# Kernel tuning notes

Measured on AMD Instinct MI355X. Metric: run time of the kernel, lower is better.

The kernel has to match this reference:

```python
import jax, jax.numpy as jnp
import numpy as np
import math

NUM_HEADS = 16
HEAD_SIZE = 64
BLOCK = 64          # SLA block size for pooled block scores / sparse selection
TOPK_RATIO = 0.1    # fraction of KV blocks attended per query block


def setup_inputs() -> dict:
    key = jax.random.key(0)
    kq, kk, kv = jax.random.split(key, 3)
    B, S, HD = 2, 4096, NUM_HEADS * HEAD_SIZE
    return {
        "query": jax.random.normal(kq, (B, S, HD), dtype=jnp.float32),
        "key": jax.random.normal(kk, (B, S, HD), dtype=jnp.float32),
        "value": jax.random.normal(kv, (B, S, HD), dtype=jnp.float32),
    }


def _sla_attention(q, k, v):
    # q, k, v: (B, H, S, D). Block-topk sparse attention (SLA-style):
    # mean-pool q/k per block, score blocks, keep top-k key blocks per
    # query block, gather only those K/V blocks, softmax over them.
    B, H, S, D = q.shape
    Nb = S // BLOCK
    scale = 1.0 / math.sqrt(D)

    qb = q.reshape(B, H, Nb, BLOCK, D)
    kb = k.reshape(B, H, Nb, BLOCK, D)
    vb = v.reshape(B, H, Nb, BLOCK, D)

    q_pool = qb.mean(axis=3)  # (B,H,Nb,D)
    k_pool = kb.mean(axis=3)  # (B,H,Nb,D)
    block_scores = jnp.einsum("bhid,bhjd->bhij", q_pool, k_pool) * scale

    K = max(1, int(math.ceil(TOPK_RATIO * Nb)))
    _, idx = jax.lax.top_k(block_scores, K)  # (B,H,Nb,K) selected key blocks

    # Gather selected key/value blocks: (B,H,Nb,K,BLOCK,D)
    gather_idx = idx[..., None, None]
    k_sel = jnp.take_along_axis(kb[:, :, None], gather_idx, axis=3)
    v_sel = jnp.take_along_axis(vb[:, :, None], gather_idx, axis=3)

    # Per-query-block scores over the K*BLOCK selected keys
    scores = jnp.einsum("bhnqd,bhnkjd->bhnqkj", qb, k_sel) * scale
    scores = scores.reshape(B, H, Nb, BLOCK, K * BLOCK)
    probs = jax.nn.softmax(scores, axis=-1)

    v_flat = v_sel.reshape(B, H, Nb, K * BLOCK, D)
    out = jnp.einsum("bhnqk,bhnkd->bhnqd", probs, v_flat)
    return out.reshape(B, H, S, D)


def reference(query, key, value):
    B, S, HD = query.shape
    H, D = NUM_HEADS, HEAD_SIZE
    # b s (h d) -> b h s d
    q = query.reshape(B, S, H, D).transpose(0, 2, 1, 3)
    k = key.reshape(B, S, H, D).transpose(0, 2, 1, 3)
    v = value.reshape(B, S, H, D).transpose(0, 2, 1, 3)
    out = _sla_attention(q, k, v)  # (B,H,S,D)
    # b h s d -> b s (h d)
    return out.transpose(0, 2, 1, 3).reshape(B, S, HD)
```

## Files before the change

### kernel.cpp

```cpp
#include <hip/hip_runtime.h>

constexpr int Bn = 2;
constexpr int Sn = 4096;
constexpr int Hh = 16;
constexpr int Dn = 64;
constexpr int HD = 1024;
constexpr int NB = 64;
constexpr int KS = 7;

typedef _Float16 f16x8 __attribute__((ext_vector_type(8)));
typedef _Float16 f16x4 __attribute__((ext_vector_type(4)));
typedef float    f32x4 __attribute__((ext_vector_type(4)));

static __device__ __forceinline__ f16x4 cvt4(float4 v) {
    f16x4 r;
    r[0] = (_Float16)v.x; r[1] = (_Float16)v.y;
    r[2] = (_Float16)v.z; r[3] = (_Float16)v.w;
    return r;
}
static __device__ __forceinline__ f16x8 cvt8(float4 a, float4 b) {
    f16x8 r;
    r[0] = (_Float16)a.x; r[1] = (_Float16)a.y;
    r[2] = (_Float16)a.z; r[3] = (_Float16)a.w;
    r[4] = (_Float16)b.x; r[5] = (_Float16)b.y;
    r[6] = (_Float16)b.z; r[7] = (_Float16)b.w;
    return r;
}

__global__ __launch_bounds__(64) void sla_pool(const float* __restrict__ Q,
                                               const float* __restrict__ K,
                                               float* __restrict__ qpool,
                                               float* __restrict__ kpool) {
    int bid = blockIdx.x;
    int b   = bid / (Hh * NB);
    int rem = bid % (Hh * NB);
    int h   = rem / NB;
    int nb  = rem % NB;
    int d   = threadIdx.x;

    const float* qp = Q + ((size_t)b * Sn + (size_t)nb * 64) * HD + h * Dn + d;
    const float* kp = K + ((size_t)b * Sn + (size_t)nb * 64) * HD + h * Dn + d;
    double sq = 0.0, sk = 0.0;
    #pragma unroll 16
    for (int r = 0; r < 64; ++r) {
        sq += (double)qp[(size_t)r * HD];
        sk += (double)kp[(size_t)r * HD];
    }
    qpool[(size_t)bid * 64 + d] = (float)(sq * (1.0 / 64.0));
    kpool[(size_t)bid * 64 + d] = (float)(sk * (1.0 / 64.0));
}

__global__ __launch_bounds__(64) void sla_topk(const float* __restrict__ qpool,
                                               const float* __restrict__ kpool,
                                               int* __restrict__ topk) {
    int bid = blockIdx.x;
    int bh  = bid / NB;
    int j   = threadIdx.x;

    const float* qp = qpool + (size_t)bid * 64;
    const float* kp = kpool + ((size_t)bh * NB + j) * 64;
    double s = 0.0;
    #pragma unroll 8
    for (int d = 0; d < 64; ++d) s += (double)qp[d] * (double)kp[d];

    double v  = s;
    int   idx = j;
    #pragma unroll
    for (int it = 0; it < KS; ++it) {
        double bv = v; int bi = idx;
        #pragma unroll
        for (int off = 1; off < 64; off <<= 1) {
            double ov = __shfl_xor(bv, off);
            int    oi = __shfl_xor(bi, off);
            if (ov > bv || (ov == bv && oi < bi)) { bv = ov; bi = oi; }
        }
        if (j == 0) topk[(size_t)bid * KS + it] = bi;
        if (idx == bi) v = -1e300;
    }
}

__global__ __launch_bounds__(256) void sla_attn(const float* __restrict__ Q,
                                                const float* __restrict__ K,
                                                const float* __restrict__ V,
                                                const int* __restrict__ topk,
                                                float* __restrict__ O) {
    __shared__ _Float16 Ks[64][64];
    __shared__ _Float16 Vt[64][72];
    __shared__ _Float16 Pq[4][16][68];

    int raw = blockIdx.x;
    int bid = (raw & 7) * 256 + (raw >> 3);

    int b   = bid / (Hh * NB);
    int rem = bid % (Hh * NB);
    int h   = rem / NB;
    int nb  = rem % NB;

    int tid  = threadIdx.x;
    int w    = tid >> 6;
    int lane = tid & 63;
    int c    = lane & 15;
    int g    = lane >> 4;

    int skey = tid >> 2;
    int sd3  = tid & 3;
    int sdg  = sd3 << 4;
    int vcol = skey ^ (sd3 << 4);
    int kch0 = ((sd3 << 1) + 0) ^ (skey & 7);
    int kch1 = ((sd3 << 1) + 1) ^ (skey & 7);
    int rch0 = (g + 0) ^ (c & 7);
    int rch1 = (g + 4) ^ (c & 7);

    int jidx[KS];
    {
        const int* tkp = topk + (size_t)bid * KS;
        #pragma unroll
        for (int i = 0; i < KS; ++i) jidx[i] = tkp[i];
    }

    f16x8 qf[2];
    {
        const float* qrow = Q + ((size_t)b * Sn + (size_t)nb * 64 + w * 16 + c) * HD + h * Dn;
        #pragma unroll
        for (int s2 = 0; s2 < 2; ++s2) {
            float4 a0 = *(const float4*)(qrow + s2 * 32 + g * 8);
            float4 a1 = *(const float4*)(qrow + s2 * 32 + g * 8 + 4);
            f16x8 q;
            q[0] = (_Float16)(a0.x * 0.125f); q[1] = (_Float16)(a0.y * 0.125f);
            q[2] = (_Float16)(a0.z * 0.125f); q[3] = (_Float16)(a0.w * 0.125f);
            q[4] = (_Float16)(a1.x * 0.125f); q[5] = (_Float16)(a1.y * 0.125f);
            q[6] = (_Float16)(a1.z * 0.125f); q[7] = (_Float16)(a1.w * 0.125f);
            qf[s2] = q;
        }
    }

    float m = -1e30f, l = 0.f;
    f32x4 oacc[4];
    #pragma unroll
    for (int t = 0; t < 4; ++t) oacc[t] = f32x4{0.f, 0.f, 0.f, 0.f};

    const float* kbase = K + (size_t)b * Sn * HD + h * Dn;
    const float* vbase = V + (size_t)b * Sn * HD + h * Dn;

    float4 kx[4], vx[4];
    {
        const float* kp = kbase + ((size_t)jidx[0] * 64 + skey) * HD + sdg;
        const float* vp = vbase + ((size_t)jidx[0] * 64 + skey) * HD + sdg;
        #pragma unroll
        for (int i = 0; i < 4; ++i) kx[i] = *(const float4*)(kp + i * 4);
        #pragma unroll
        for (int i = 0; i < 4; ++i) vx[i] = *(const float4*)(vp + i * 4);
    }

    for (int kb = 0; kb < KS; ++kb) {
        __syncthreads();
        *(f16x8*)&Ks[skey][kch0 * 8] = cvt8(kx[0], kx[1]);
        *(f16x8*)&Ks[skey][kch1 * 8] = cvt8(kx[2], kx[3]);
        #pragma unroll
        for (int i = 0; i < 4; ++i) {
            float4 v = vx[i];
            int db = sdg + i * 4;
            Vt[db + 0][vcol] = (_Float16)v.x;
            Vt[db + 1][vcol] = (_Float16)v.y;
            Vt[db + 2][vcol] = (_Float16)v.z;
            Vt[db + 3][vcol] = (_Float16)v.w;
        }
        if (kb + 1 < KS) {
            const float* kp = kbase + ((size_t)jidx[kb + 1] * 64 + skey) * HD + sdg;
            const float* vp = vbase + ((size_t)jidx[kb + 1] * 64 + skey) * HD + sdg;
            #pragma unroll
            for (int i = 0; i < 4; ++i) kx[i] = *(const float4*)(kp + i * 4);
            #pragma unroll
            for (int i = 0; i < 4; ++i) vx[i] = *(const float4*)(vp + i * 4);
        }
        __syncthreads();

        f32x4 sacc[4];
        #pragma unroll
        for (int t = 0; t < 4; ++t) sacc[t] = f32x4{0.f, 0.f, 0.f, 0.f};
        #pragma unroll
        for (int t = 0; t < 4; ++t) {
            f16x8 a0 = *(const f16x8*)&Ks[t * 16 + c][rch0 * 8];
            f16x8 a1 = *(const f16x8*)&Ks[t * 16 + c][rch1 * 8];
            sacc[t] = __builtin_amdgcn_mfma_f32_16x16x32_f16(a0, qf[0], sacc[t], 0, 0, 0);
            sacc[t] = __builtin_amdgcn_mfma_f32_16x16x32_f16(a1, qf[1], sacc[t], 0, 0, 0);
        }

        float pm;
        {
            float m0 = fmaxf(fmaxf(sacc[0][0], sacc[0][1]), fmaxf(sacc[0][2], sacc[0][3]));
            float m1 = fmaxf(fmaxf(sacc[1][0], sacc[1][1]), fmaxf(sacc[1][2], sacc[1][3]));
            float m2 = fmaxf(fmaxf(sacc[2][0], sacc[2][1]), fmaxf(sacc[2][2], sacc[2][3]));
            float m3 = fmaxf(fmaxf(sacc[3][0], sacc[3][1]), fmaxf(sacc[3][2], sacc[3][3]));
            pm = fmaxf(fmaxf(m0, m1), fmaxf(m2, m3));
        }
        pm = fmaxf(pm, __shfl_xor(pm, 16));
        pm = fmaxf(pm, __shfl_xor(pm, 32));

        float mn = fmaxf(m, pm);
        float al = __expf(m - mn);
        m = mn;

        float e[4][4];
        float rs = 0.f;
        #pragma unroll
        for (int t = 0; t < 4; ++t) {
            #pragma unroll
            for (int r = 0; r < 4; ++r) {
                float x = __expf(sacc[t][r] - m);
                e[t][r] = x;
                rs += x;
            }
        }
        rs += __shfl_xor(rs, 16);
        rs += __shfl_xor(rs, 32);
        l = l * al + rs;
        #pragma unroll
        for (int t = 0; t < 4; ++t) {
            oacc[t][0] *= al; oacc[t][1] *= al;
            oacc[t][2] *= al; oacc[t][3] *= al;
        }

        #pragma unroll
        for (int t = 0; t < 4; ++t) {
            f16x4 p4;
            p4[0] = (_Float16)e[t][0]; p4[1] = (_Float16)e[t][1];
            p4[2] = (_Float16)e[t][2]; p4[3] = (_Float16)e[t][3];
            *(f16x4*)&Pq[w][c][t * 16 + g * 4] = p4;
        }

        #pragma unroll
        for (int t = 0; t < 4; ++t) {
            int cv0 = (g * 8)      ^ ((t & 3) << 4);
            int cv1 = (32 + g * 8) ^ ((t & 3) << 4);
            f16x8 va0 = *(const f16x8*)&Vt[t * 16 + c][cv0];
            f16x8 va1 = *(const f16x8*)&Vt[t * 16 + c][cv1];
            f16x8 pa0 = *(const f16x8*)&Pq[w][c][g * 8];
            f16x8 pa1 = *(const f16x8*)&Pq[w][c][32 + g * 8];
            oacc[t] = __builtin_amdgcn_mfma_f32_16x16x32_f16(va0, pa0, oacc[t], 0, 0, 0);
            oacc[t] = __builtin_amdgcn_mfma_f32_16x16x32_f16(va1, pa1, oacc[t], 0, 0, 0);
        }
    }

    float inv = 1.0f / l;
    float* orow = O + ((size_t)b * Sn + (size_t)nb * 64 + w * 16 + c) * HD + h * Dn;
    #pragma unroll
    for (int t = 0; t < 4; ++t) {
        float4 o4;
        o4.x = oacc[t][0] * inv; o4.y = oacc[t][1] * inv;
        o4.z = oacc[t][2] * inv; o4.w = oacc[t][3] * inv;
        *(float4*)(orow + t * 16 + g * 4) = o4;
    }
}

extern "C" void kernel_launch(void* const* d_in, const int* in_sizes, int n_in,
                              void* d_out, int out_size, void* d_ws, size_t ws_size,
                              hipStream_t stream) {
    const float* Q = (const float*)d_in[0];
    const float* K = (const float*)d_in[1];
    const float* V = (const float*)d_in[2];
    float* O = (float*)d_out;

    float* qpool = (float*)d_ws;
    float* kpool = qpool + (size_t)Bn * Hh * NB * Dn;
    int*   topk  = (int*)(kpool + (size_t)Bn * Hh * NB * Dn);

    dim3 grid(Bn * Hh * NB);
    sla_pool<<<grid, 64, 0, stream>>>(Q, K, qpool, kpool);
    sla_topk<<<grid, 64, 0, stream>>>(qpool, kpool, topk);
    sla_attn<<<grid, 256, 0, stream>>>(Q, K, V, topk, O);
}
```

Baseline: 73.59 us.

## Double-buffer K/V LDS tiles, vectorize pooling, use exp2 softmax with packed conversions

The attention kernel now double-buffers the K and V^T shared-memory tiles. This needs one barrier per iteration instead of two, and global loads are issued two blocks ahead. The loop is fully unrolled, and s_setprio is raised around the MFMA sections. The softmax switches to exp2 by folding log2(e) into the Q scale, and probabilities are packed to fp16 with cvt_pkrtz, which rounds toward zero and slightly changes precision. The pooling kernel is rewritten to use float4 loads across 4 row groups with shuffle reductions. The Vt padding is removed, which relies on the XOR swizzle to avoid bank conflicts.

```diff
diff --git a/kernel.cpp b/kernel.cpp
--- a/kernel.cpp
+++ b/kernel.cpp
@@ -10,14 +10,15 @@
 
 typedef _Float16 f16x8 __attribute__((ext_vector_type(8)));
 typedef _Float16 f16x4 __attribute__((ext_vector_type(4)));
+typedef _Float16 f16x2 __attribute__((ext_vector_type(2)));
+typedef __fp16   hf2   __attribute__((ext_vector_type(2)));
 typedef float    f32x4 __attribute__((ext_vector_type(4)));
 
-static __device__ __forceinline__ f16x4 cvt4(float4 v) {
-    f16x4 r;
-    r[0] = (_Float16)v.x; r[1] = (_Float16)v.y;
-    r[2] = (_Float16)v.z; r[3] = (_Float16)v.w;
-    return r;
-}
+#define BARRIER_LDS() do { \
+    asm volatile("s_waitcnt lgkmcnt(0)" ::: "memory"); \
+    __builtin_amdgcn_s_barrier(); \
+} while (0)
+
 static __device__ __forceinline__ f16x8 cvt8(float4 a, float4 b) {
     f16x8 r;
     r[0] = (_Float16)a.x; r[1] = (_Float16)a.y;
@@ -27,27 +28,50 @@
     return r;
 }
 
+static __device__ __forceinline__ f16x2 pkrtz(float a, float b) {
+    hf2 t = __builtin_amdgcn_cvt_pkrtz(a, b);
+    return __builtin_bit_cast(f16x2, t);
+}
+
 __global__ __launch_bounds__(64) void sla_pool(const float* __restrict__ Q,
                                                const float* __restrict__ K,
                                                float* __restrict__ qpool,
                                                float* __restrict__ kpool) {
-    int bid = blockIdx.x;
-    int b   = bid / (Hh * NB);
-    int rem = bid % (Hh * NB);
-    int h   = rem / NB;
-    int nb  = rem % NB;
-    int d   = threadIdx.x;
-
-    const float* qp = Q + ((size_t)b * Sn + (size_t)nb * 64) * HD + h * Dn + d;
-    const float* kp = K + ((size_t)b * Sn + (size_t)nb * 64) * HD + h * Dn + d;
-    double sq = 0.0, sk = 0.0;
-    #pragma unroll 16
-    for (int r = 0; r < 64; ++r) {
-        sq += (double)qp[(size_t)r * HD];
-        sk += (double)kp[(size_t)r * HD];
-    }
-    qpool[(size_t)bid * 64 + d] = (float)(sq * (1.0 / 64.0));
-    kpool[(size_t)bid * 64 + d] = (float)(sk * (1.0 / 64.0));
+    int bid  = blockIdx.x;
+    int b    = bid / (Hh * NB);
+    int rem  = bid % (Hh * NB);
+    int h    = rem / NB;
+    int nb   = rem % NB;
+    int tid  = threadIdx.x;
+    int quad = tid >> 4;
+    int dq   = (tid & 15) << 2;
+
+    const float* qb = Q + ((size_t)b * Sn + (size_t)nb * 64) * HD + h * Dn + dq;
+    const float* kb = K + ((size_t)b * Sn + (size_t)nb * 64) * HD + h * Dn + dq;
+
+    double sq[4] = {0, 0, 0, 0}, sk[4] = {0, 0, 0, 0};
+    #pragma unroll
+    for (int i = 0; i < 16; ++i) {
+        size_t off = (size_t)(quad + i * 4) * HD;
+        float4 x = *(const float4*)(qb + off);
+        float4 y = *(const float4*)(kb + off);
+        sq[0] += x.x; sq[1] += x.y; sq[2] += x.z; sq[3] += x.w;
+        sk[0] += y.x; sk[1] += y.y; sk[2] += y.z; sk[3] += y.w;
+    }
+    #pragma unroll
+    for (int j = 0; j < 4; ++j) {
+        sq[j] += __shfl_xor(sq[j], 16); sq[j] += __shfl_xor(sq[j], 32);
+        sk[j] += __shfl_xor(sk[j], 16); sk[j] += __shfl_xor(sk[j], 32);
+    }
+    if (quad == 0) {
+        float4 oq, ok;
+        oq.x = (float)(sq[0] * (1.0 / 64.0)); oq.y = (float)(sq[1] * (1.0 / 64.0));
+        oq.z = (float)(sq[2] * (1.0 / 64.0)); oq.w = (float)(sq[3] * (1.0 / 64.0));
+        ok.x = (float)(sk[0] * (1.0 / 64.0)); ok.y = (float)(sk[1] * (1.0 / 64.0));
+        ok.z = (float)(sk[2] * (1.0 / 64.0)); ok.w = (float)(sk[3] * (1.0 / 64.0));
+        *(float4*)(qpool + (size_t)bid * 64 + dq) = oq;
+        *(float4*)(kpool + (size_t)bid * 64 + dq) = ok;
+    }
 }
 
 __global__ __launch_bounds__(64) void sla_topk(const float* __restrict__ qpool,
@@ -84,8 +108,8 @@
                                                 const float* __restrict__ V,
                                                 const int* __restrict__ topk,
                                                 float* __restrict__ O) {
-    __shared__ _Float16 Ks[64][64];
-    __shared__ _Float16 Vt[64][72];
+    __shared__ _Float16 Ks[2][64][64];
+    __shared__ _Float16 Vt[2][64][64];
     __shared__ _Float16 Pq[4][16][68];
 
     int raw = blockIdx.x;
@@ -118,6 +142,7 @@
         for (int i = 0; i < KS; ++i) jidx[i] = tkp[i];
     }
 
+    const float QS = 0.18033688f;
     f16x8 qf[2];
     {
         const float* qrow = Q + ((size_t)b * Sn + (size_t)nb * 64 + w * 16 + c) * HD + h * Dn;
@@ -126,10 +151,10 @@
             float4 a0 = *(const float4*)(qrow + s2 * 32 + g * 8);
             float4 a1 = *(const float4*)(qrow + s2 * 32 + g * 8 + 4);
             f16x8 q;
-            q[0] = (_Float16)(a0.x * 0.125f); q[1] = (_Float16)(a0.y * 0.125f);
-            q[2] = (_Float16)(a0.z * 0.125f); q[3] = (_Float16)(a0.w * 0.125f);
-            q[4] = (_Float16)(a1.x * 0.125f); q[5] = (_Float16)(a1.y * 0.125f);
-            q[6] = (_Float16)(a1.z * 0.125f); q[7] = (_Float16)(a1.w * 0.125f);
+            q[0] = (_Float16)(a0.x * QS); q[1] = (_Float16)(a0.y * QS);
+            q[2] = (_Float16)(a0.z * QS); q[3] = (_Float16)(a0.w * QS);
+            q[4] = (_Float16)(a1.x * QS); q[5] = (_Float16)(a1.y * QS);
+            q[6] = (_Float16)(a1.z * QS); q[7] = (_Float16)(a1.w * QS);
             qf[s2] = q;
         }
     }
@@ -143,48 +168,49 @@
     const float* vbase = V + (size_t)b * Sn * HD + h * Dn;
 
     float4 kx[4], vx[4];
-    {
-        const float* kp = kbase + ((size_t)jidx[0] * 64 + skey) * HD + sdg;
-        const float* vp = vbase + ((size_t)jidx[0] * 64 + skey) * HD + sdg;
+    auto LOAD = [&](int blk) {
+        const float* kp = kbase + ((size_t)blk * 64 + skey) * HD + sdg;
+        const float* vp = vbase + ((size_t)blk * 64 + skey) * HD + sdg;
         #pragma unroll
         for (int i = 0; i < 4; ++i) kx[i] = *(const float4*)(kp + i * 4);
         #pragma unroll
         for (int i = 0; i < 4; ++i) vx[i] = *(const float4*)(vp + i * 4);
-    }
-
-    for (int kb = 0; kb < KS; ++kb) {
-        __syncthreads();
-        *(f16x8*)&Ks[skey][kch0 * 8] = cvt8(kx[0], kx[1]);
-        *(f16x8*)&Ks[skey][kch1 * 8] = cvt8(kx[2], kx[3]);
+    };
+    auto STAGE = [&](int buf) {
+        *(f16x8*)&Ks[buf][skey][kch0 * 8] = cvt8(kx[0], kx[1]);
+        *(f16x8*)&Ks[buf][skey][kch1 * 8] = cvt8(kx[2], kx[3]);
         #pragma unroll
         for (int i = 0; i < 4; ++i) {
             float4 v = vx[i];
             int db = sdg + i * 4;
-            Vt[db + 0][vcol] = (_Float16)v.x;
-            Vt[db + 1][vcol] = (_Float16)v.y;
-            Vt[db + 2][vcol] = (_Float16)v.z;
-            Vt[db + 3][vcol] = (_Float16)v.w;
-        }
-        if (kb + 1 < KS) {
-            const float* kp = kbase + ((size_t)jidx[kb + 1] * 64 + skey) * HD + sdg;
-            const float* vp = vbase + ((size_t)jidx[kb + 1] * 64 + skey) * HD + sdg;
-            #pragma unroll
-            for (int i = 0; i < 4; ++i) kx[i] = *(const float4*)(kp + i * 4);
-            #pragma unroll
-            for (int i = 0; i < 4; ++i) vx[i] = *(const float4*)(vp + i * 4);
-        }
-        __syncthreads();
+            Vt[buf][db + 0][vcol] = (_Float16)v.x;
+            Vt[buf][db + 1][vcol] = (_Float16)v.y;
+            Vt[buf][db + 2][vcol] = (_Float16)v.z;
+            Vt[buf][db + 3][vcol] = (_Float16)v.w;
+        }
+    };
+
+    LOAD(jidx[0]);
+    STAGE(0);
+    LOAD(jidx[1]);
+    BARRIER_LDS();
+
+    #pragma unroll
+    for (int kb = 0; kb < KS; ++kb) {
+        const int cur = kb & 1;
 
         f32x4 sacc[4];
         #pragma unroll
         for (int t = 0; t < 4; ++t) sacc[t] = f32x4{0.f, 0.f, 0.f, 0.f};
-        #pragma unroll
-        for (int t = 0; t < 4; ++t) {
-            f16x8 a0 = *(const f16x8*)&Ks[t * 16 + c][rch0 * 8];
-            f16x8 a1 = *(const f16x8*)&Ks[t * 16 + c][rch1 * 8];
+        __builtin_amdgcn_s_setprio(1);
+        #pragma unroll
+        for (int t = 0; t < 4; ++t) {
+            f16x8 a0 = *(const f16x8*)&Ks[cur][t * 16 + c][rch0 * 8];
+            f16x8 a1 = *(const f16x8*)&Ks[cur][t * 16 + c][rch1 * 8];
             sacc[t] = __builtin_amdgcn_mfma_f32_16x16x32_f16(a0, qf[0], sacc[t], 0, 0, 0);
             sacc[t] = __builtin_amdgcn_mfma_f32_16x16x32_f16(a1, qf[1], sacc[t], 0, 0, 0);
         }
+        __builtin_amdgcn_s_setprio(0);
 
         float pm;
         {
@@ -198,7 +224,7 @@
         pm = fmaxf(pm, __shfl_xor(pm, 32));
 
         float mn = fmaxf(m, pm);
-        float al = __expf(m - mn);
+        float al = __builtin_amdgcn_exp2f(m - mn);
         m = mn;
 
         float e[4][4];
@@ -207,7 +233,7 @@
         for (int t = 0; t < 4; ++t) {
             #pragma unroll
             for (int r = 0; r < 4; ++r) {
-                float x = __expf(sacc[t][r] - m);
+                float x = __builtin_amdgcn_exp2f(sacc[t][r] - m);
                 e[t][r] = x;
                 rs += x;
             }
@@ -223,22 +249,31 @@
 
         #pragma unroll
         for (int t = 0; t < 4; ++t) {
+            f16x2 lo = pkrtz(e[t][0], e[t][1]);
+            f16x2 hi = pkrtz(e[t][2], e[t][3]);
             f16x4 p4;
-            p4[0] = (_Float16)e[t][0]; p4[1] = (_Float16)e[t][1];
-            p4[2] = (_Float16)e[t][2]; p4[3] = (_Float16)e[t][3];
+            p4[0] = lo[0]; p4[1] = lo[1]; p4[2] = hi[0]; p4[3] = hi[1];
             *(f16x4*)&Pq[w][c][t * 16 + g * 4] = p4;
         }
 
-        #pragma unroll
-        for (int t = 0; t < 4; ++t) {
-            int cv0 = (g * 8)      ^ ((t & 3) << 4);
-            int cv1 = (32 + g * 8) ^ ((t & 3) << 4);
-            f16x8 va0 = *(const f16x8*)&Vt[t * 16 + c][cv0];
-            f16x8 va1 = *(const f16x8*)&Vt[t * 16 + c][cv1];
-            f16x8 pa0 = *(const f16x8*)&Pq[w][c][g * 8];
-            f16x8 pa1 = *(const f16x8*)&Pq[w][c][32 + g * 8];
+        f16x8 pa0 = *(const f16x8*)&Pq[w][c][g * 8];
+        f16x8 pa1 = *(const f16x8*)&Pq[w][c][32 + g * 8];
+        __builtin_amdgcn_s_setprio(1);
+        #pragma unroll
+        for (int t = 0; t < 4; ++t) {
+            int cv0 = (g * 8)      ^ (t << 4);
+            int cv1 = (32 + g * 8) ^ (t << 4);
+            f16x8 va0 = *(const f16x8*)&Vt[cur][t * 16 + c][cv0];
+            f16x8 va1 = *(const f16x8*)&Vt[cur][t * 16 + c][cv1];
             oacc[t] = __builtin_amdgcn_mfma_f32_16x16x32_f16(va0, pa0, oacc[t], 0, 0, 0);
             oacc[t] = __builtin_amdgcn_mfma_f32_16x16x32_f16(va1, pa1, oacc[t], 0, 0, 0);
+        }
+        __builtin_amdgcn_s_setprio(0);
+
+        if (kb + 1 < KS) {
+            STAGE(cur ^ 1);
+            if (kb + 2 < KS) LOAD(jidx[kb + 2]);
+            BARRIER_LDS();
         }
     }
 
```

Measured after the change: 79.59 us. 8.2% more time.
